# Kernel tuning notes

Measured on AMD Instinct MI355X. Metric: run time of the kernel, lower is better.

Reference implementation:

```python
import jax, jax.numpy as jnp
import numpy as np

EMBED = 1024
HEADS = 16
HEAD_DIM = EMBED // HEADS
T = 1024
B = 2
TEMP = 1.0
EPS = 1e-20


def setup_inputs() -> dict:
    key = jax.random.key(0)
    ks = jax.random.split(key, 8)
    s = 0.02  # xavier-ish init scale
    return {
        "g": jax.random.normal(ks[0], (T, B, EMBED), dtype=jnp.float32),
        "h": jax.random.normal(ks[1], (T, B, EMBED), dtype=jnp.float32),
        "g_in_w": jax.random.normal(ks[2], (3 * EMBED, EMBED), dtype=jnp.float32) * s,
        "g_in_b": jnp.zeros((3 * EMBED,), dtype=jnp.float32),
        "h_in_w": jax.random.normal(ks[3], (2 * EMBED, EMBED), dtype=jnp.float32) * s,
        "h_in_b": jnp.zeros((2 * EMBED,), dtype=jnp.float32),
        "g_out_w": jax.random.normal(ks[4], (EMBED, EMBED), dtype=jnp.float32) * s,
        "g_out_b": jnp.zeros((EMBED,), dtype=jnp.float32),
        "h_out_w": jax.random.normal(ks[5], (EMBED, EMBED), dtype=jnp.float32) * s,
        "h_out_b": jnp.zeros((EMBED,), dtype=jnp.float32),
    }


def reference(g, h, g_in_w, g_in_b, h_in_w, h_in_b, g_out_w, g_out_b, h_out_w, h_out_b):
    Tt, Bb, E = g.shape
    H, d = HEADS, HEAD_DIM

    # fused qkv projection on g stream, kv on h stream (F.linear: x @ W^T + b)
    q, gk, gv = jnp.split(g @ g_in_w.T + g_in_b, 3, axis=-1)
    hk, hv = jnp.split(h @ h_in_w.T + h_in_b, 2, axis=-1)
    q = q * (d ** -0.5)

    def to_heads(x):  # [T,B,E] -> [B,H,T,d]
        return x.reshape(Tt, Bb, H, d).transpose(1, 2, 0, 3)

    q, gk, gv, hk, hv = map(to_heads, (q, gk, gv, hk, hv))

    # dual-stream attention scores
    g_scores = jnp.einsum("bhtd,bhsd->bhts", q, gk)
    h_scores = jnp.einsum("bhtd,bhsd->bhts", q, hk)

    g_p = jax.nn.softmax(g_scores, axis=-1)
    h_p = jax.nn.softmax(h_scores, axis=-1)

    # gumbel-softmax sample of h_scores (mode='gumbel', temperature=TEMP)
    u = jax.random.uniform(jax.random.key(42), h_scores.shape, dtype=h_scores.dtype)
    noise = -jnp.log(-jnp.log(u + EPS) + EPS)
    sample = jax.nn.softmax((jax.nn.log_softmax(h_scores, axis=-1) + noise) / TEMP, axis=-1)

    g_attn = jnp.einsum("bhts,bhsd->bhtd", g_p, gv)
    h_attn = jnp.einsum("bhts,bhsd->bhtd", sample, hv)

    def merge(x):  # [B,H,T,d] -> [T,B,E]
        return x.transpose(2, 0, 1, 3).reshape(Tt, Bb, E)

    g_out = merge(g_attn) @ g_out_w.T + g_out_b
    h_out = merge(h_attn) @ h_out_w.T + h_out_b
    return g_out, h_out
```

## Files before the change

### kernel.cpp

```cpp
#include <hip/hip_runtime.h>
#include <stdint.h>

#define T_SEQ 1024

typedef __attribute__((ext_vector_type(8))) short short8;
typedef __attribute__((ext_vector_type(4))) float f32x4;
typedef __attribute__((ext_vector_type(4))) unsigned short ushort4v;
typedef __attribute__((ext_vector_type(8))) unsigned short ushort8v;

__device__ __forceinline__ unsigned short f2bf(float f) {
  union { float f; uint32_t u; } v; v.f = f;
  return (unsigned short)((v.u + 0x7fffu + ((v.u >> 16) & 1u)) >> 16);
}
__device__ __forceinline__ float bf2f(unsigned short u) {
  union { uint32_t u; float f; } v; v.u = ((uint32_t)u) << 16;
  return v.f;
}

__device__ __forceinline__ void gl2lds16(const unsigned short* g, unsigned short* l) {
  __builtin_amdgcn_global_load_lds(
      (const __attribute__((address_space(1))) void*)g,
      (__attribute__((address_space(3))) void*)l, 16, 0, 0);
}

__device__ __forceinline__ uint32_t tf_bits(uint32_t flat) {
  const uint32_t ks1 = 42u;
  const uint32_t ks2 = 0x1BD11BDAu ^ 42u;
  uint32_t x0 = 0u;
  uint32_t x1 = flat + ks1;
#define TFR(r) { x0 += x1; x1 = (x1 << (r)) | (x1 >> (32 - (r))); x1 ^= x0; }
  TFR(13) TFR(15) TFR(26) TFR(6)
  x0 += ks1; x1 += ks2 + 1u;
  TFR(17) TFR(29) TFR(16) TFR(24)
  x0 += ks2; x1 += 2u;
  TFR(13) TFR(15) TFR(26) TFR(6)
  x1 += ks1 + 3u;
  TFR(17) TFR(29) TFR(16) TFR(24)
  x0 += ks1; x1 += ks2 + 4u;
  TFR(13) TFR(15) TFR(26) TFR(6)
  x0 += ks2; x1 += 5u;
#undef TFR
  return x0 ^ x1;
}

__device__ __forceinline__ float gumbel_noise(uint32_t flat) {
  const uint32_t bits = tf_bits(flat);
  const float u = __uint_as_float((bits >> 9) | 0x3f800000u) - 1.0f;
  return -__logf(-__logf(u + 1e-20f) + 1e-20f);
}

__global__ __launch_bounds__(256) void convert_pre(
    const float* __restrict__ g, const float* __restrict__ h,
    const float* __restrict__ wgi_f, const float* __restrict__ whi_f,
    const float* __restrict__ wgo_f, const float* __restrict__ who_f,
    unsigned short* __restrict__ gbf, unsigned short* __restrict__ hbf,
    unsigned short* __restrict__ wgi, unsigned short* __restrict__ whi,
    unsigned short* __restrict__ wgo, unsigned short* __restrict__ who)
{
  const int64_t Q_SPLIT = 1048576;
  const int64_t Q_TOTAL = Q_SPLIT + 1835008;
  for (int64_t qd = (int64_t)blockIdx.x * 256 + threadIdx.x; qd < Q_TOTAL;
       qd += (int64_t)gridDim.x * 256) {
    if (qd < Q_SPLIT) {
      const int which = qd >= 524288;
      const int64_t e = (qd - (which ? 524288 : 0)) * 4;
      const float4 v = *(const float4*)((which ? h : g) + e);
      ushort4v u = {f2bf(v.x), f2bf(v.y), f2bf(v.z), f2bf(v.w)};
      *(ushort4v*)((which ? hbf : gbf) + e) = u;
    } else {
      int64_t off = qd - Q_SPLIT;
      const float* src; unsigned short* dst;
      if (off < 786432)                 { src = wgi_f; dst = wgi; }
      else if (off < 1310720)           { off -= 786432;  src = whi_f; dst = whi; }
      else if (off < 1572864)           { off -= 1310720; src = wgo_f; dst = wgo; }
      else                              { off -= 1572864; src = who_f; dst = who; }
      const int64_t e = off * 4;
      const float4 v = *(const float4*)(src + e);
      ushort4v u = {f2bf(v.x), f2bf(v.y), f2bf(v.z), f2bf(v.w)};
      *(ushort4v*)(dst + e) = u;
    }
  }
}

template<int TM, bool BF16OUT>
__device__ __forceinline__ void gemm_plain_core(
    const unsigned short* __restrict__ Ab, const unsigned short* __restrict__ Wb,
    const float* __restrict__ bias, int N, int K, int m0, int n0,
    int scale_limit, void* Cout, unsigned short* sA, unsigned short* sW)
{
  const int tid = threadIdx.x;
  const int w = tid >> 6;
  const int lane = tid & 63;
  const int txl = lane & 15, q = lane >> 4;
  const int wr = (w >> 1) * (TM * 16);
  const int wc = (w & 1) << 6;
  const int lr = lane >> 3, lu = lane & 7;
  const int rx7 = txl & 7;

  const unsigned short* Asrc = Ab + (size_t)(m0 + w * 8 * TM + lr) * K + ((lu ^ lr) << 3);
  const unsigned short* Wsrc = Wb + (size_t)(n0 + w * 32 + lr) * K + ((lu ^ lr) << 3);
  unsigned short* sAd = sA + (w * 8 * TM) * 64;
  unsigned short* sWd = sW + (w * 32) * 64;

  f32x4 acc[TM][4];
#pragma unroll
  for (int i = 0; i < TM; i++)
#pragma unroll
    for (int j = 0; j < 4; j++) acc[i][j] = (f32x4){0.f, 0.f, 0.f, 0.f};

  for (int k0 = 0; k0 < K; k0 += 64) {
    __syncthreads();
#pragma unroll
    for (int i = 0; i < TM; i++)
      gl2lds16(Asrc + (size_t)(8 * i) * K + k0, sAd + (8 * i) * 64);
#pragma unroll
    for (int i = 0; i < 4; i++)
      gl2lds16(Wsrc + (size_t)(8 * i) * K + k0, sWd + (8 * i) * 64);
    __syncthreads();
#pragma unroll
    for (int kk = 0; kk < 2; kk++) {
      const int uoff = ((4 * kk + q) ^ rx7) << 3;
      short8 af[TM], wf[4];
#pragma unroll
      for (int i = 0; i < TM; i++)
        af[i] = *(const short8*)&sA[(wr + 16 * i + txl) * 64 + uoff];
#pragma unroll
      for (int j = 0; j < 4; j++)
        wf[j] = *(const short8*)&sW[(wc + 16 * j + txl) * 64 + uoff];
#pragma unroll
      for (int i = 0; i < TM; i++)
#pragma unroll
        for (int j = 0; j < 4; j++)
          acc[i][j] = __builtin_amdgcn_mfma_f32_16x16x32_bf16(af[i], wf[j], acc[i][j], 0, 0, 0);
    }
  }

#pragma unroll
  for (int j = 0; j < 4; j++) {
    const int col = n0 + wc + 16 * j + txl;
    const float bj = bias[col];
    const float sc = (col < scale_limit) ? 0.125f : 1.0f;
#pragma unroll
    for (int i = 0; i < TM; i++) {
      const int rbase = m0 + wr + 16 * i + 4 * q;
#pragma unroll
      for (int r = 0; r < 4; r++) {
        const float v = (acc[i][j][r] + bj) * sc;
        if (BF16OUT) ((unsigned short*)Cout)[(size_t)(rbase + r) * N + col] = f2bf(v);
        else         ((float*)Cout)[(size_t)(rbase + r) * N + col] = v;
      }
    }
  }
}

__global__ __launch_bounds__(256, 4) void gemm_inproj(
    const unsigned short* __restrict__ gbf, const unsigned short* __restrict__ wgi,
    const float* __restrict__ bgi,
    const unsigned short* __restrict__ hbf, const unsigned short* __restrict__ whi,
    const float* __restrict__ bhi,
    unsigned short* __restrict__ qkv, unsigned short* __restrict__ hkv)
{
  __shared__ __align__(16) unsigned short sm[16384];
  const int bx = blockIdx.x;
  const int m0 = blockIdx.y * 128;
  if (bx < 24)
    gemm_plain_core<4, true>(gbf, wgi, bgi, 3072, 1024, m0, bx * 128, 1024,
                             qkv, sm, sm + 8192);
  else
    gemm_plain_core<4, true>(hbf, whi, bhi, 2048, 1024, m0, (bx - 24) * 128, 0,
                             hkv, sm, sm + 8192);
}

__global__ __launch_bounds__(256, 2) void gemm_outproj(
    const unsigned short* __restrict__ attnb,
    const unsigned short* __restrict__ wgo, const float* __restrict__ bgo,
    const unsigned short* __restrict__ who, const float* __restrict__ bho,
    float* __restrict__ out)
{
  __shared__ __align__(16) unsigned short sm[12288];
  const int m0 = blockIdx.y * 64;
  const unsigned short* Wp = (m0 < 2048) ? wgo : who;
  const float* bp = (m0 < 2048) ? bgo : bho;
  gemm_plain_core<2, false>(attnb, Wp, bp, 1024, 1024, m0, blockIdx.x * 128, 0,
                            out, sm, sm + 4096);
}

__global__ __launch_bounds__(256) void transpose_v(
    const unsigned short* __restrict__ qkv, const unsigned short* __restrict__ hkv,
    unsigned short* __restrict__ vTg, unsigned short* __restrict__ vTh)
{
  __shared__ __align__(16) unsigned short sm[64 * 72];
  const int tid = threadIdx.x;
  const int t0 = blockIdx.x * 64;
  const int d0 = blockIdx.y * 64;
  const int zb = blockIdx.z;
  const int b = zb & 1;
  const int strm = zb >> 1;
  const unsigned short* src = strm ? hkv : qkv;
  const int srcoff = strm ? 1024 : 2048;
  const int sstride = strm ? 2048 : 3072;
  unsigned short* dst = strm ? vTh : vTg;

  const int r = tid >> 2, cs = (tid & 3) << 4;
  {
    const size_t gsrc = (size_t)((t0 + r) * 2 + b) * sstride + srcoff + d0 + cs;
    *(ushort8v*)&sm[r * 72 + cs]     = *(const ushort8v*)&src[gsrc];
    *(ushort8v*)&sm[r * 72 + cs + 8] = *(const ushort8v*)&src[gsrc + 8];
  }
  __syncthreads();
  const int dr = tid >> 2, ts = (tid & 3) << 4;
  ushort8v o0, o1;
#pragma unroll
  for (int m = 0; m < 8; m++) o0[m] = sm[(ts + m) * 72 + dr];
#pragma unroll
  for (int m = 0; m < 8; m++) o1[m] = sm[(ts + 8 + m) * 72 + dr];
  const size_t gdst = (size_t)b * 1048576 + (size_t)(d0 + dr) * 1024 + t0 + ts;
  *(ushort8v*)&dst[gdst]     = o0;
  *(ushort8v*)&dst[gdst + 8] = o1;
}

__global__ __launch_bounds__(256, 3) void attn_mfma(
    const unsigned short* __restrict__ qkv, const unsigned short* __restrict__ hkv,
    const unsigned short* __restrict__ vTg, const unsigned short* __restrict__ vTh,
    float* __restrict__ Opart, float* __restrict__ lpart)
{
  __shared__ __align__(16) unsigned short smem[25600];
  unsigned short* KB = smem;
  unsigned short* VB = smem + 8192;
  unsigned short* PC = smem + 16384;
  unsigned short* QS = smem;

  const int tid = threadIdx.x;
  const int w = tid >> 6;
  const int lane = tid & 63;
  const int txl = lane & 15, q = lane >> 4;
  const int rx7 = txl & 7;
  const int lr = lane >> 3, lu = lane & 7;
  const int su = (lu ^ lr) << 3;
  const int t0 = blockIdx.x * 64;
  const int bh = blockIdx.y;
  const int z = blockIdx.z;
  const int b = bh >> 4;
  const int head = bh & 15;
  const int hoff = head * 64;
  const int sr = tid >> 2;
  const int sc = (tid & 3) << 4;

  {
    const size_t gq = ((size_t)(t0 + sr) * 2 + b) * 3072 + hoff + sc;
    *(ushort8v*)&QS[sr * 72 + sc]     = *(const ushort8v*)&qkv[gq];
    *(ushort8v*)&QS[sr * 72 + sc + 8] = *(const ushort8v*)&qkv[gq + 8];
  }
  __syncthreads();
  const short8 aq0 = *(const short8*)&QS[(16 * w + txl) * 72 + 8 * q];
  const short8 aq1 = *(const short8*)&QS[(16 * w + txl) * 72 + 32 + 8 * q];

  f32x4 Og[4], Oh[4];
  float l_g[4], l_h[4];
#pragma unroll
  for (int i = 0; i < 4; i++) {
    Og[i] = (f32x4){0.f, 0.f, 0.f, 0.f};
    Oh[i] = (f32x4){0.f, 0.f, 0.f, 0.f};
    l_g[i] = 0.f; l_h[i] = 0.f;
  }

  unsigned short* pcg = PC + (w * 2 + 0) * 1152;
  unsigned short* pch = PC + (w * 2 + 1) * 1152;
  const unsigned short* vTgb = vTg + (size_t)b * 1048576;
  const unsigned short* vThb = vTh + (size_t)b * 1048576;

  const int u0 = (q ^ rx7) << 3;
  const int u1 = ((4 + q) ^ rx7) << 3;
  const f32x4 zz = (f32x4){0.f, 0.f, 0.f, 0.f};

  const int s_begin = z * (T_SEQ / 2);
  const int s_end = s_begin + (T_SEQ / 2);
  for (int s0 = s_begin; s0 < s_end; s0 += 64) {
    __syncthreads();
#pragma unroll
    for (int t = 0; t < 2; t++) {
      const int rb = w * 16 + 8 * t;
      const size_t krow = (size_t)(s0 + rb + lr) * 2 + b;
      gl2lds16(&qkv[krow * 3072 + 1024 + hoff + su], &KB[rb * 64]);
      gl2lds16(&hkv[krow * 2048 +        hoff + su], &KB[4096 + rb * 64]);
      const size_t vrow = (size_t)(hoff + rb + lr) * 1024 + s0 + su;
      gl2lds16(&vTgb[vrow], &VB[rb * 64]);
      gl2lds16(&vThb[vrow], &VB[4096 + rb * 64]);
    }
    float ng[4][4];
#pragma unroll
    for (int nt = 0; nt < 4; nt++)
#pragma unroll
      for (int r = 0; r < 4; r++) {
        const uint32_t trow = (uint32_t)(t0 + 16 * w + 4 * q + r);
        const uint32_t scol_ = (uint32_t)(s0 + 16 * nt + txl);
        ng[nt][r] = gumbel_noise(((uint32_t)bh << 20) | (trow << 10) | scol_);
      }
    __syncthreads();

    f32x4 Sg[4], Sh[4];
    __builtin_amdgcn_s_setprio(1);
#pragma unroll
    for (int nt = 0; nt < 4; nt++) {
      const int srw = (16 * nt + txl) * 64;
      const short8 bg0 = *(const short8*)&KB[srw + u0];
      const short8 bg1 = *(const short8*)&KB[srw + u1];
      const short8 bh0 = *(const short8*)&KB[4096 + srw + u0];
      const short8 bh1 = *(const short8*)&KB[4096 + srw + u1];
      f32x4 ag = __builtin_amdgcn_mfma_f32_16x16x32_bf16(aq0, bg0, zz, 0, 0, 0);
      ag = __builtin_amdgcn_mfma_f32_16x16x32_bf16(aq1, bg1, ag, 0, 0, 0);
      f32x4 ah = __builtin_amdgcn_mfma_f32_16x16x32_bf16(aq0, bh0, zz, 0, 0, 0);
      ah = __builtin_amdgcn_mfma_f32_16x16x32_bf16(aq1, bh1, ah, 0, 0, 0);
      Sg[nt] = ag; Sh[nt] = ah;
    }
    __builtin_amdgcn_s_setprio(0);

#pragma unroll
    for (int nt = 0; nt < 4; nt++) {
      float eg[4], eh[4];
#pragma unroll
      for (int r = 0; r < 4; r++) {
        eg[r] = __expf(Sg[nt][r]);             l_g[r] += eg[r];
        eh[r] = __expf(Sh[nt][r] + ng[nt][r]); l_h[r] += eh[r];
      }
      const int sbase = (16 * nt + txl) * 18 + 4 * q;
      *(uint32_t*)&pcg[sbase]     = (uint32_t)f2bf(eg[0]) | ((uint32_t)f2bf(eg[1]) << 16);
      *(uint32_t*)&pcg[sbase + 2] = (uint32_t)f2bf(eg[2]) | ((uint32_t)f2bf(eg[3]) << 16);
      *(uint32_t*)&pch[sbase]     = (uint32_t)f2bf(eh[0]) | ((uint32_t)f2bf(eh[1]) << 16);
      *(uint32_t*)&pch[sbase + 2] = (uint32_t)f2bf(eh[2]) | ((uint32_t)f2bf(eh[3]) << 16);
    }

    short8 apg[2], aph[2];
#pragma unroll
    for (int c = 0; c < 2; c++)
#pragma unroll
      for (int j = 0; j < 8; j++) {
        apg[c][j] = (short)pcg[(32 * c + 8 * q + j) * 18 + txl];
        aph[c][j] = (short)pch[(32 * c + 8 * q + j) * 18 + txl];
      }

    __builtin_amdgcn_s_setprio(1);
#pragma unroll
    for (int c = 0; c < 2; c++) {
      const int uv = (c == 0) ? u0 : u1;
#pragma unroll
      for (int nt = 0; nt < 4; nt++) {
        const int drw = (16 * nt + txl) * 64;
        const short8 bvg = *(const short8*)&VB[drw + uv];
        const short8 bvh = *(const short8*)&VB[4096 + drw + uv];
        Og[nt] = __builtin_amdgcn_mfma_f32_16x16x32_bf16(apg[c], bvg, Og[nt], 0, 0, 0);
        Oh[nt] = __builtin_amdgcn_mfma_f32_16x16x32_bf16(aph[c], bvh, Oh[nt], 0, 0, 0);
      }
    }
    __builtin_amdgcn_s_setprio(0);
  }

  float* opg = Opart + ((size_t)(z * 2 + 0) * 2048) * 1024;
  float* oph = Opart + ((size_t)(z * 2 + 1) * 2048) * 1024;
  float* lpg = lpart + (size_t)(z * 2 + 0) * 2048 * 16;
  float* lph = lpart + (size_t)(z * 2 + 1) * 2048 * 16;
#pragma unroll
  for (int r = 0; r < 4; r++) {
    float lg = l_g[r], lh = l_h[r];
    lg += __shfl_xor(lg, 1); lg += __shfl_xor(lg, 2);
    lg += __shfl_xor(lg, 4); lg += __shfl_xor(lg, 8);
    lh += __shfl_xor(lh, 1); lh += __shfl_xor(lh, 2);
    lh += __shfl_xor(lh, 4); lh += __shfl_xor(lh, 8);
    const int row = (t0 + 16 * w + 4 * q + r) * 2 + b;
    if (txl == 0) {
      lpg[row * 16 + head] = lg;
      lph[row * 16 + head] = lh;
    }
    const size_t base = (size_t)row * 1024 + hoff;
#pragma unroll
    for (int nt = 0; nt < 4; nt++) {
      opg[base + 16 * nt + txl] = Og[nt][r];
      oph[base + 16 * nt + txl] = Oh[nt][r];
    }
  }
}

__global__ __launch_bounds__(256) void merge_attn(
    const float* __restrict__ Opart, const float* __restrict__ lpart,
    unsigned short* __restrict__ attnb)
{
  const int idx = blockIdx.x * 256 + threadIdx.x;
  const int st = idx >> 19;
  const int i = idx & 0x7FFFF;
  const int row = i >> 8;
  const int colq = i & 255;
  const int head = colq >> 4;
  const float4 o0 = *(const float4*)&Opart[((size_t)(0 + st) * 2048 + row) * 1024 + colq * 4];
  const float4 o1 = *(const float4*)&Opart[((size_t)(2 + st) * 2048 + row) * 1024 + colq * 4];
  const float l0 = lpart[(size_t)(0 + st) * 32768 + row * 16 + head];
  const float l1 = lpart[(size_t)(2 + st) * 32768 + row * 16 + head];
  const float inv = 1.0f / (l0 + l1);
  ushort4v u = {f2bf((o0.x + o1.x) * inv), f2bf((o0.y + o1.y) * inv),
                f2bf((o0.z + o1.z) * inv), f2bf((o0.w + o1.w) * inv)};
  *(ushort4v*)&attnb[((size_t)st * 2048 + row) * 1024 + colq * 4] = u;
}

extern "C" void kernel_launch(void* const* d_in, const int* in_sizes, int n_in,
                              void* d_out, int out_size, void* d_ws, size_t ws_size,
                              hipStream_t stream) {
  const float* g       = (const float*)d_in[0];
  const float* h       = (const float*)d_in[1];
  const float* g_in_w  = (const float*)d_in[2];
  const float* g_in_b  = (const float*)d_in[3];
  const float* h_in_w  = (const float*)d_in[4];
  const float* h_in_b  = (const float*)d_in[5];
  const float* g_out_w = (const float*)d_in[6];
  const float* g_out_b = (const float*)d_in[7];
  const float* h_out_w = (const float*)d_in[8];
  const float* h_out_b = (const float*)d_in[9];
  float* out = (float*)d_out;

  unsigned short* ws = (unsigned short*)d_ws;
  unsigned short* qkv   = ws;
  unsigned short* hkv   = qkv + (size_t)2048*3072;
  unsigned short* attnb = hkv + (size_t)2048*2048;
  unsigned short* wgo   = attnb + (size_t)4096*1024;
  unsigned short* who   = wgo + (size_t)1024*1024;
  unsigned short* scratch = who + (size_t)1024*1024;
  unsigned short* gbf = scratch;
  unsigned short* hbf = gbf + (size_t)2048*1024;
  unsigned short* wgi = hbf + (size_t)2048*1024;
  unsigned short* whi = wgi + (size_t)3072*1024;
  float* Opart = (float*)scratch;
  float* lpart = Opart + (size_t)4*2048*1024;
  unsigned short* vTg = (unsigned short*)(lpart + (size_t)4*2048*16);
  unsigned short* vTh = vTg + (size_t)2*1024*1024;

  convert_pre<<<1024, 256, 0, stream>>>(g, h, g_in_w, h_in_w, g_out_w, h_out_w,
                                        gbf, hbf, wgi, whi, wgo, who);
  gemm_inproj<<<dim3(40, 16), 256, 0, stream>>>(
      gbf, wgi, g_in_b, hbf, whi, h_in_b, qkv, hkv);
  transpose_v<<<dim3(16, 16, 4), 256, 0, stream>>>(qkv, hkv, vTg, vTh);
  attn_mfma<<<dim3(T_SEQ / 64, 32, 2), 256, 0, stream>>>(qkv, hkv, vTg, vTh, Opart, lpart);
  merge_attn<<<4096, 256, 0, stream>>>(Opart, lpart, attnb);
  gemm_outproj<<<dim3(8, 64), 256, 0, stream>>>(
      attnb, wgo, g_out_b, who, h_out_b, out);
}
```

Baseline: 267.2 us.

## Drop split-K attention and normalize output directly in attention kernel

```diff
diff --git a/kernel.cpp b/kernel.cpp
--- a/kernel.cpp
+++ b/kernel.cpp
@@ -222,7 +222,7 @@
 __global__ __launch_bounds__(256, 3) void attn_mfma(
     const unsigned short* __restrict__ qkv, const unsigned short* __restrict__ hkv,
     const unsigned short* __restrict__ vTg, const unsigned short* __restrict__ vTh,
-    float* __restrict__ Opart, float* __restrict__ lpart)
+    unsigned short* __restrict__ attnb)
 {
   __shared__ __align__(16) unsigned short smem[25600];
   unsigned short* KB = smem;
@@ -239,7 +239,6 @@
   const int su = (lu ^ lr) << 3;
   const int t0 = blockIdx.x * 64;
   const int bh = blockIdx.y;
-  const int z = blockIdx.z;
   const int b = bh >> 4;
   const int head = bh & 15;
   const int hoff = head * 64;
@@ -273,9 +272,7 @@
   const int u1 = ((4 + q) ^ rx7) << 3;
   const f32x4 zz = (f32x4){0.f, 0.f, 0.f, 0.f};
 
-  const int s_begin = z * (T_SEQ / 2);
-  const int s_end = s_begin + (T_SEQ / 2);
-  for (int s0 = s_begin; s0 < s_end; s0 += 64) {
+  for (int s0 = 0; s0 < T_SEQ; s0 += 64) {
     __syncthreads();
 #pragma unroll
     for (int t = 0; t < 2; t++) {
@@ -355,10 +352,8 @@
     __builtin_amdgcn_s_setprio(0);
   }
 
-  float* opg = Opart + ((size_t)(z * 2 + 0) * 2048) * 1024;
-  float* oph = Opart + ((size_t)(z * 2 + 1) * 2048) * 1024;
-  float* lpg = lpart + (size_t)(z * 2 + 0) * 2048 * 16;
-  float* lph = lpart + (size_t)(z * 2 + 1) * 2048 * 16;
+  unsigned short* abg = attnb;
+  unsigned short* abh = attnb + (size_t)2048 * 1024;
 #pragma unroll
   for (int r = 0; r < 4; r++) {
     float lg = l_g[r], lh = l_h[r];
@@ -366,38 +361,16 @@
     lg += __shfl_xor(lg, 4); lg += __shfl_xor(lg, 8);
     lh += __shfl_xor(lh, 1); lh += __shfl_xor(lh, 2);
     lh += __shfl_xor(lh, 4); lh += __shfl_xor(lh, 8);
+    const float ivg = 1.0f / lg;
+    const float ivh = 1.0f / lh;
     const int row = (t0 + 16 * w + 4 * q + r) * 2 + b;
-    if (txl == 0) {
-      lpg[row * 16 + head] = lg;
-      lph[row * 16 + head] = lh;
-    }
     const size_t base = (size_t)row * 1024 + hoff;
 #pragma unroll
     for (int nt = 0; nt < 4; nt++) {
-      opg[base + 16 * nt + txl] = Og[nt][r];
-      oph[base + 16 * nt + txl] = Oh[nt][r];
-    }
-  }
-}
-
-__global__ __launch_bounds__(256) void merge_attn(
-    const float* __restrict__ Opart, const float* __restrict__ lpart,
-    unsigned short* __restrict__ attnb)
-{
-  const int idx = blockIdx.x * 256 + threadIdx.x;
-  const int st = idx >> 19;
-  const int i = idx & 0x7FFFF;
-  const int row = i >> 8;
-  const int colq = i & 255;
-  const int head = colq >> 4;
-  const float4 o0 = *(const float4*)&Opart[((size_t)(0 + st) * 2048 + row) * 1024 + colq * 4];
-  const float4 o1 = *(const float4*)&Opart[((size_t)(2 + st) * 2048 + row) * 1024 + colq * 4];
-  const float l0 = lpart[(size_t)(0 + st) * 32768 + row * 16 + head];
-  const float l1 = lpart[(size_t)(2 + st) * 32768 + row * 16 + head];
-  const float inv = 1.0f / (l0 + l1);
-  ushort4v u = {f2bf((o0.x + o1.x) * inv), f2bf((o0.y + o1.y) * inv),
-                f2bf((o0.z + o1.z) * inv), f2bf((o0.w + o1.w) * inv)};
-  *(ushort4v*)&attnb[((size_t)st * 2048 + row) * 1024 + colq * 4] = u;
+      abg[base + 16 * nt + txl] = f2bf(Og[nt][r] * ivg);
+      abh[base + 16 * nt + txl] = f2bf(Oh[nt][r] * ivh);
+    }
+  }
 }
 
 extern "C" void kernel_launch(void* const* d_in, const int* in_sizes, int n_in,
@@ -426,9 +399,8 @@
   unsigned short* hbf = gbf + (size_t)2048*1024;
   unsigned short* wgi = hbf + (size_t)2048*1024;
   unsigned short* whi = wgi + (size_t)3072*1024;
-  float* Opart = (float*)scratch;
-  float* lpart = Opart + (size_t)4*2048*1024;
-  unsigned short* vTg = (unsigned short*)(lpart + (size_t)4*2048*16);
+  float* rsv = (float*)scratch;
+  unsigned short* vTg = (unsigned short*)(rsv + (size_t)4*2048*1024 + (size_t)4*2048*16);
   unsigned short* vTh = vTg + (size_t)2*1024*1024;
 
   convert_pre<<<1024, 256, 0, stream>>>(g, h, g_in_w, h_in_w, g_out_w, h_out_w,
@@ -436,8 +408,7 @@
   gemm_inproj<<<dim3(40, 16), 256, 0, stream>>>(
       gbf, wgi, g_in_b, hbf, whi, h_in_b, qkv, hkv);
   transpose_v<<<dim3(16, 16, 4), 256, 0, stream>>>(qkv, hkv, vTg, vTh);
-  attn_mfma<<<dim3(T_SEQ / 64, 32, 2), 256, 0, stream>>>(qkv, hkv, vTg, vTh, Opart, lpart);
-  merge_attn<<<4096, 256, 0, stream>>>(Opart, lpart, attnb);
+  attn_mfma<<<dim3(T_SEQ / 64, 32), 256, 0, stream>>>(qkv, hkv, vTg, vTh, attnb);
   gemm_outproj<<<dim3(8, 64), 256, 0, stream>>>(
       attnb, wgo, g_out_b, who, h_out_b, out);
 }
```

Measured after the change: 268.7 us. About the same (+0.6%).
